# Performance work log

Measured on AMD Instinct MI355X. Metric: run time of the kernel, lower is better.

The kernel has to match this reference:

```python
import jax, jax.numpy as jnp
import numpy as np

KH, KW = 3, 3
DIL = 1
PH = DIL * (KH - 1) // 2
PW = DIL * (KW - 1) // 2


def setup_inputs() -> dict:
    key = jax.random.key(0)
    kq, kk = jax.random.split(key)
    B, C, H, W = 8, 128, 128, 128
    Q = jax.random.normal(kq, (B, C, H, W), dtype=jnp.float32)
    K = jax.random.normal(kk, (B, C, H, W), dtype=jnp.float32)
    return {"Q": Q, "K": K}


def reference(Q, K):
    # output[b, i*KW+j, h, w] = sum_c Q[b,c,h,w] * K_padded[b,c,h+i*DIL, w+j*DIL]
    B, C, H, W = Q.shape
    Kp = jnp.pad(K, ((0, 0), (0, 0), (PH, PH), (PW, PW)))
    outs = []
    for i in range(KH):
        for j in range(KW):
            Ks = Kp[:, :, i * DIL:i * DIL + H, j * DIL:j * DIL + W]  # shifted K window
            outs.append(jnp.sum(Q * Ks, axis=1))  # reduce over channels -> (B,H,W)
    return jnp.stack(outs, axis=1)  # (B, KH*KW, H, W)
```

## Files before the change

kernel.cpp:

```cpp
#include <hip/hip_runtime.h>


#define Bn 8
#define Cn 128
#define Hn 128
#define Wn 128
#define HWn (Hn * Wn)
#define ROWS 32
#define CSPLIT 8
#define CCHUNK (Cn / CSPLIT)
#define OUTN (Bn * 9 * HWn)

template <bool ATOMIC>
__global__ __launch_bounds__(1024) void msa_conv_v6(
    const float* __restrict__ Q, const float* __restrict__ K,
    float* __restrict__ dst) {
  const int idx = threadIdx.x;
  const int wq  = idx & 31;
  const int rr  = idx >> 5;
  const int w0  = wq * 4;
  const int r   = blockIdx.x * ROWS + rr;
  const int b   = blockIdx.y;
  const int cs  = blockIdx.z;

  const int rm = (r > 0) ? r - 1 : r + 1;
  const int rp = (r < Hn - 1) ? r + 1 : r - 1;

  const size_t base = ((size_t)b * Cn + (size_t)cs * CCHUNK) * HWn;
  const float* qp = Q + base + (size_t)r  * Wn + w0;
  const float* mp = K + base + (size_t)rm * Wn + w0;
  const float* zp = K + base + (size_t)r  * Wn + w0;
  const float* pp = K + base + (size_t)rp * Wn + w0;

  float acc[9][4] = {};

#define ACC4(t, s0, s1, s2, s3) \
  acc[t][0] += q4.x * (s0);     \
  acc[t][1] += q4.y * (s1);     \
  acc[t][2] += q4.z * (s2);     \
  acc[t][3] += q4.w * (s3);

#pragma unroll 4
  for (int c = 0; c < CCHUNK; ++c) {
    const float4 q4 = *(const float4*)qp;
    const float4 m4 = *(const float4*)mp;
    const float4 z4 = *(const float4*)zp;
    const float4 p4 = *(const float4*)pp;
    const float mL = __shfl_up(m4.w, 1, 64);
    const float zL = __shfl_up(z4.w, 1, 64);
    const float pL = __shfl_up(p4.w, 1, 64);
    const float mR = __shfl_down(m4.x, 1, 64);
    const float zR = __shfl_down(z4.x, 1, 64);
    const float pR = __shfl_down(p4.x, 1, 64);

    ACC4(0, mL,   m4.x, m4.y, m4.z)
    ACC4(1, m4.x, m4.y, m4.z, m4.w)
    ACC4(2, m4.y, m4.z, m4.w, mR)
    ACC4(3, zL,   z4.x, z4.y, z4.z)
    ACC4(4, z4.x, z4.y, z4.z, z4.w)
    ACC4(5, z4.y, z4.z, z4.w, zR)
    ACC4(6, pL,   p4.x, p4.y, p4.z)
    ACC4(7, p4.x, p4.y, p4.z, p4.w)
    ACC4(8, p4.y, p4.z, p4.w, pR)

    qp += HWn; mp += HWn; zp += HWn; pp += HWn;
  }
#undef ACC4

  if (wq == 0)  { acc[0][0] = 0.f; acc[3][0] = 0.f; acc[6][0] = 0.f; }
  if (wq == 31) { acc[2][3] = 0.f; acc[5][3] = 0.f; acc[8][3] = 0.f; }
  if (r == 0) {
#pragma unroll
    for (int t = 0; t < 3; ++t)
#pragma unroll
      for (int k = 0; k < 4; ++k) acc[t][k] = 0.f;
  }
  if (r == Hn - 1) {
#pragma unroll
    for (int t = 6; t < 9; ++t)
#pragma unroll
      for (int k = 0; k < 4; ++k) acc[t][k] = 0.f;
  }

  const size_t o = (size_t)b * 9 * HWn + (size_t)r * Wn + w0;
  if (ATOMIC) {
#pragma unroll
    for (int t = 0; t < 9; ++t)
#pragma unroll
      for (int k = 0; k < 4; ++k)
        atomicAdd(dst + o + (size_t)t * HWn + k, acc[t][k]);
  } else {
    float* p = dst + (size_t)cs * OUTN + o;
#pragma unroll
    for (int t = 0; t < 9; ++t)
      *(float4*)(p + (size_t)t * HWn) =
          make_float4(acc[t][0], acc[t][1], acc[t][2], acc[t][3]);
  }
}

__global__ __launch_bounds__(256) void msa_reduce8(
    const float* __restrict__ part, float* __restrict__ out) {
  const int i = blockIdx.x * 256 + threadIdx.x;
  const int n4 = OUTN / 4;
  const float4* p = (const float4*)part;
  float4 s = p[i];
#pragma unroll
  for (int cs = 1; cs < CSPLIT; ++cs) {
    const float4 v = p[(size_t)cs * n4 + i];
    s.x += v.x; s.y += v.y; s.z += v.z; s.w += v.w;
  }
  ((float4*)out)[i] = s;
}

__global__ __launch_bounds__(256) void msa_zero(float* __restrict__ out) {
  const int i = blockIdx.x * 256 + threadIdx.x;
  ((float4*)out)[i] = make_float4(0.f, 0.f, 0.f, 0.f);
}

extern "C" void kernel_launch(void* const* d_in, const int* in_sizes, int n_in,
                              void* d_out, int out_size, void* d_ws,
                              size_t ws_size, hipStream_t stream) {
  const float* Q = (const float*)d_in[0];
  const float* K = (const float*)d_in[1];
  float* out = (float*)d_out;

  dim3 block(1024);
  dim3 grid(Hn / ROWS, Bn, CSPLIT);

  const size_t ws_need = (size_t)CSPLIT * OUTN * sizeof(float);
  if (ws_size >= ws_need) {
    float* part = (float*)d_ws;
    msa_conv_v6<false><<<grid, block, 0, stream>>>(Q, K, part);
    msa_reduce8<<<OUTN / 4 / 256, 256, 0, stream>>>(part, out);
  } else {
    msa_zero<<<OUTN / 4 / 256, 256, 0, stream>>>(out);
    msa_conv_v6<true><<<grid, block, 0, stream>>>(Q, K, out);
  }
}
```

Before: 162.6 us.

## Move channel-split reduction into shared memory within one fused kernel

Each 512-thread block now covers two rows of one batch and splits the 128 channels across eight 64-thread groups. The groups combine their 36 partial sums per thread through a tree reduction in a double-buffered shared array, and group 0 writes the final output directly. This drops the partial-sum workspace, its write and re-read through global memory, and the separate reduce kernel launch. In exchange it adds several block-wide barriers with idle groups, fully unrolls the 16-channel loop, and launches a different grid shape.

```diff
diff --git a/kernel.cpp b/kernel.cpp
--- a/kernel.cpp
+++ b/kernel.cpp
@@ -6,27 +6,28 @@
 #define Hn 128
 #define Wn 128
 #define HWn (Hn * Wn)
-#define ROWS 32
-#define CSPLIT 8
-#define CCHUNK (Cn / CSPLIT)
-#define OUTN (Bn * 9 * HWn)
+#define NG 8
+#define CG (Cn / NG)
 
-template <bool ATOMIC>
-__global__ __launch_bounds__(1024) void msa_conv_v6(
+__global__ __launch_bounds__(512, 4) void msa_conv_v7(
     const float* __restrict__ Q, const float* __restrict__ K,
-    float* __restrict__ dst) {
-  const int idx = threadIdx.x;
-  const int wq  = idx & 31;
-  const int rr  = idx >> 5;
+    float* __restrict__ out) {
+  __shared__ float buf[2][36][65];
+
+  const int tid = threadIdx.x;
+  const int cg  = tid >> 6;
+  const int s   = tid & 63;
+  const int wq  = s & 31;
+  const int rr  = s >> 5;
   const int w0  = wq * 4;
-  const int r   = blockIdx.x * ROWS + rr;
+  const int r0  = blockIdx.x * 2;
+  const int r   = r0 + rr;
   const int b   = blockIdx.y;
-  const int cs  = blockIdx.z;
 
   const int rm = (r > 0) ? r - 1 : r + 1;
   const int rp = (r < Hn - 1) ? r + 1 : r - 1;
 
-  const size_t base = ((size_t)b * Cn + (size_t)cs * CCHUNK) * HWn;
+  const size_t base = ((size_t)b * Cn + (size_t)cg * CG) * HWn;
   const float* qp = Q + base + (size_t)r  * Wn + w0;
   const float* mp = K + base + (size_t)rm * Wn + w0;
   const float* zp = K + base + (size_t)r  * Wn + w0;
@@ -40,8 +41,8 @@
   acc[t][2] += q4.z * (s2);     \
   acc[t][3] += q4.w * (s3);
 
-#pragma unroll 4
-  for (int c = 0; c < CCHUNK; ++c) {
+#pragma unroll
+  for (int c = 0; c < CG; ++c) {
     const float4 q4 = *(const float4*)qp;
     const float4 m4 = *(const float4*)mp;
     const float4 z4 = *(const float4*)zp;
@@ -67,54 +68,65 @@
   }
 #undef ACC4
 
-  if (wq == 0)  { acc[0][0] = 0.f; acc[3][0] = 0.f; acc[6][0] = 0.f; }
-  if (wq == 31) { acc[2][3] = 0.f; acc[5][3] = 0.f; acc[8][3] = 0.f; }
-  if (r == 0) {
+#define WRITE(p)                                              \
+  do {                                                        \
+    _Pragma("unroll") for (int t = 0; t < 9; ++t)             \
+    _Pragma("unroll") for (int k = 0; k < 4; ++k)             \
+        buf[p][t * 4 + k][s] = acc[t][k];                     \
+  } while (0)
+#define ADD(p)                                                \
+  do {                                                        \
+    _Pragma("unroll") for (int t = 0; t < 9; ++t)             \
+    _Pragma("unroll") for (int k = 0; k < 4; ++k)             \
+        acc[t][k] += buf[p][t * 4 + k][s];                    \
+  } while (0)
+
+  if (cg == 4) WRITE(0);
+  if (cg == 5) WRITE(1);
+  __syncthreads();
+  if (cg == 0) ADD(0);
+  if (cg == 1) ADD(1);
+  __syncthreads();
+  if (cg == 6) WRITE(0);
+  if (cg == 7) WRITE(1);
+  __syncthreads();
+  if (cg == 2) ADD(0);
+  if (cg == 3) ADD(1);
+  __syncthreads();
+  if (cg == 2) WRITE(0);
+  if (cg == 3) WRITE(1);
+  __syncthreads();
+  if (cg == 0) ADD(0);
+  if (cg == 1) ADD(1);
+  __syncthreads();
+  if (cg == 1) WRITE(0);
+  __syncthreads();
+
+  if (cg == 0) {
+    ADD(0);
+    if (wq == 0)  { acc[0][0] = 0.f; acc[3][0] = 0.f; acc[6][0] = 0.f; }
+    if (wq == 31) { acc[2][3] = 0.f; acc[5][3] = 0.f; acc[8][3] = 0.f; }
+    if (r == 0) {
 #pragma unroll
-    for (int t = 0; t < 3; ++t)
+      for (int t = 0; t < 3; ++t)
 #pragma unroll
-      for (int k = 0; k < 4; ++k) acc[t][k] = 0.f;
-  }
-  if (r == Hn - 1) {
+        for (int k = 0; k < 4; ++k) acc[t][k] = 0.f;
+    }
+    if (r == Hn - 1) {
 #pragma unroll
-    for (int t = 6; t < 9; ++t)
+      for (int t = 6; t < 9; ++t)
 #pragma unroll
-      for (int k = 0; k < 4; ++k) acc[t][k] = 0.f;
-  }
+        for (int k = 0; k < 4; ++k) acc[t][k] = 0.f;
+    }
 
-  const size_t o = (size_t)b * 9 * HWn + (size_t)r * Wn + w0;
-  if (ATOMIC) {
+    float* o = out + (size_t)b * 9 * HWn + (size_t)r * Wn + w0;
 #pragma unroll
     for (int t = 0; t < 9; ++t)
-#pragma unroll
-      for (int k = 0; k < 4; ++k)
-        atomicAdd(dst + o + (size_t)t * HWn + k, acc[t][k]);
-  } else {
-    float* p = dst + (size_t)cs * OUTN + o;
-#pragma unroll
-    for (int t = 0; t < 9; ++t)
-      *(float4*)(p + (size_t)t * HWn) =
+      *(float4*)(o + (size_t)t * HWn) =
           make_float4(acc[t][0], acc[t][1], acc[t][2], acc[t][3]);
   }
-}
-
-__global__ __launch_bounds__(256) void msa_reduce8(
-    const float* __restrict__ part, float* __restrict__ out) {
-  const int i = blockIdx.x * 256 + threadIdx.x;
-  const int n4 = OUTN / 4;
-  const float4* p = (const float4*)part;
-  float4 s = p[i];
-#pragma unroll
-  for (int cs = 1; cs < CSPLIT; ++cs) {
-    const float4 v = p[(size_t)cs * n4 + i];
-    s.x += v.x; s.y += v.y; s.z += v.z; s.w += v.w;
-  }
-  ((float4*)out)[i] = s;
-}
-
-__global__ __launch_bounds__(256) void msa_zero(float* __restrict__ out) {
-  const int i = blockIdx.x * 256 + threadIdx.x;
-  ((float4*)out)[i] = make_float4(0.f, 0.f, 0.f, 0.f);
+#undef WRITE
+#undef ADD
 }
 
 extern "C" void kernel_launch(void* const* d_in, const int* in_sizes, int n_in,
@@ -124,16 +136,7 @@
   const float* K = (const float*)d_in[1];
   float* out = (float*)d_out;
 
-  dim3 block(1024);
-  dim3 grid(Hn / ROWS, Bn, CSPLIT);
-
-  const size_t ws_need = (size_t)CSPLIT * OUTN * sizeof(float);
-  if (ws_size >= ws_need) {
-    float* part = (float*)d_ws;
-    msa_conv_v6<false><<<grid, block, 0, stream>>>(Q, K, part);
-    msa_reduce8<<<OUTN / 4 / 256, 256, 0, stream>>>(part, out);
-  } else {
-    msa_zero<<<OUTN / 4 / 256, 256, 0, stream>>>(out);
-    msa_conv_v6<true><<<grid, block, 0, stream>>>(Q, K, out);
-  }
+  dim3 block(512);
+  dim3 grid(Hn / 2, Bn);
+  msa_conv_v7<<<grid, block, 0, stream>>>(Q, K, out);
 }
```

Result: slower. 284.4 us (+74.9%).
